# Kernel tuning notes

Hardware: AMD Instinct MI355X
Metric: run time of the kernel (lower is better)

The kernel has to match this reference:

```python
import jax, jax.numpy as jnp
from jax import lax
import numpy as np

C_IN, C_OUT, K, STRIDE = 256, 512, 3, 1
EPS = 1e-5


def setup_inputs() -> dict:
    key = jax.random.key(0)
    ks = jax.random.split(key, 8)
    B, H, W = 32, 56, 56
    x = jax.random.normal(ks[0], (B, C_IN, H, W), dtype=jnp.float32)
    dw_w = jax.random.normal(ks[1], (C_IN, 1, K, K), dtype=jnp.float32) * 0.1
    dw_b = jax.random.normal(ks[2], (C_IN,), dtype=jnp.float32) * 0.05
    g1 = jnp.ones((C_IN,), dtype=jnp.float32)
    b1 = jnp.zeros((C_IN,), dtype=jnp.float32)
    pw_w = jax.random.normal(ks[3], (C_OUT, C_IN), dtype=jnp.float32) * (1.0 / np.sqrt(C_IN))
    pw_b = jax.random.normal(ks[4], (C_OUT,), dtype=jnp.float32) * 0.05
    g2 = jnp.ones((C_OUT,), dtype=jnp.float32)
    b2 = jnp.zeros((C_OUT,), dtype=jnp.float32)
    return {"x": x, "dw_w": dw_w, "dw_b": dw_b, "g1": g1, "b1": b1,
            "pw_w": pw_w, "pw_b": pw_b, "g2": g2, "b2": b2}


def _batchnorm(x, gamma, beta):
    # training-mode BN over (N, H, W) per channel, matching fresh nn.BatchNorm2d
    mean = jnp.mean(x, axis=(0, 2, 3), keepdims=True)
    var = jnp.var(x, axis=(0, 2, 3), keepdims=True)
    xn = (x - mean) * lax.rsqrt(var + EPS)
    return xn * gamma[None, :, None, None] + beta[None, :, None, None]


def reference(x, dw_w, dw_b, g1, b1, pw_w, pw_b, g2, b2):
    p = K // 2
    # reflect padding (padding_mode='reflect' in torch Conv2d)
    xp = jnp.pad(x, ((0, 0), (0, 0), (p, p), (p, p)), mode='reflect')
    # grouped depthwise conv: one filter per channel
    y = lax.conv_general_dilated(
        xp, dw_w, window_strides=(STRIDE, STRIDE), padding='VALID',
        dimension_numbers=('NCHW', 'OIHW', 'NCHW'),
        feature_group_count=C_IN)
    y = y + dw_b[None, :, None, None]
    y = jax.nn.relu(_batchnorm(y, g1, b1))
    # pointwise 1x1 conv == channel GEMM
    z = jnp.einsum('bchw,oc->bohw', y, pw_w) + pw_b[None, :, None, None]
    z = jax.nn.relu(_batchnorm(z, g2, b2))
    return z
```

## Files before the change

kernel.cpp:

```cpp
#include <hip/hip_runtime.h>
#include <hip/hip_bf16.h>
#include <stdint.h>


#define CIN   256
#define COUT  512
#define BATCH 32
#define HH    56
#define WWID  56
#define HWSZ  3136
#define NTOT  100352
#define NHWF  100352.0f
#define EPSV  1e-5f

typedef __bf16 bf16;
typedef __bf16 bf16x8 __attribute__((ext_vector_type(8)));
typedef float  f32x4  __attribute__((ext_vector_type(4)));

#define WS_STATS1   0
#define WS_SCALE1   2048
#define WS_SHIFT1   3072
#define WS_STATS2   4096
#define WS_WBF      16384
#define WS_YT       278528
#define WS_ZBF      51658752

__device__ __forceinline__ void gload16(const void* g, void* l) {
  __builtin_amdgcn_global_load_lds((const __attribute__((address_space(1))) void*)g,
                                   (__attribute__((address_space(3))) void*)l, 16, 0, 0);
}
__device__ __forceinline__ float bfu(unsigned int u16) {
  unsigned int x = u16 << 16;
  return __builtin_bit_cast(float, x);
}

__global__ __launch_bounds__(256) void k1_dwstats(const float* __restrict__ x,
                                                  const float* __restrict__ dww,
                                                  float* __restrict__ stats1) {
  __shared__ float plane[HWSZ];
  __shared__ float red[8];
  int bid = blockIdx.x;
  int c = bid & (CIN - 1);
  int b = bid >> 8;
  const float4* xp4 = (const float4*)(x + ((size_t)(b * CIN + c)) * HWSZ);
  float4* pl4 = (float4*)plane;
  for (int i = threadIdx.x; i < HWSZ / 4; i += 256) pl4[i] = xp4[i];
  float w9[9];
#pragma unroll
  for (int q = 0; q < 9; ++q) w9[q] = dww[c * 9 + q];
  __syncthreads();
  float s = 0.f, sq = 0.f;
  for (int p = threadIdx.x; p < HWSZ; p += 256) {
    int h = p / WWID;
    int w = p - h * WWID;
    float acc = 0.f;
#pragma unroll
    for (int dy = 0; dy < 3; ++dy) {
      int hh = h - 1 + dy;
      hh = hh < 0 ? 1 : (hh > 55 ? 54 : hh);
#pragma unroll
      for (int dx = 0; dx < 3; ++dx) {
        int ww2 = w - 1 + dx;
        ww2 = ww2 < 0 ? 1 : (ww2 > 55 ? 54 : ww2);
        acc += w9[dy * 3 + dx] * plane[hh * WWID + ww2];
      }
    }
    s += acc; sq += acc * acc;
  }
#pragma unroll
  for (int m = 1; m < 64; m <<= 1) { s += __shfl_xor(s, m); sq += __shfl_xor(sq, m); }
  int wv = threadIdx.x >> 6;
  if ((threadIdx.x & 63) == 0) { red[wv] = s; red[4 + wv] = sq; }
  __syncthreads();
  if (threadIdx.x == 0) {
    atomicAdd(&stats1[c],        red[0] + red[1] + red[2] + red[3]);
    atomicAdd(&stats1[CIN + c],  red[4] + red[5] + red[6] + red[7]);
  }
}

__global__ __launch_bounds__(256) void k2_finalize1(const float* __restrict__ stats1,
                                                    const float* __restrict__ g1,
                                                    const float* __restrict__ b1,
                                                    const float* __restrict__ pww,
                                                    float* __restrict__ scale1,
                                                    float* __restrict__ shift1,
                                                    bf16* __restrict__ wbf) {
  int blk = blockIdx.x, t = threadIdx.x;
  if (blk == 0) {
    float mean = stats1[t] * (1.0f / NHWF);
    float var  = stats1[CIN + t] * (1.0f / NHWF) - mean * mean;
    float sc = g1[t] * rsqrtf(var + EPSV);
    scale1[t] = sc;
    shift1[t] = b1[t] - mean * sc;
  } else {
    int o = blk - 1;
    wbf[o * CIN + t] = (bf16)pww[o * CIN + t];
  }
}

__global__ __launch_bounds__(256) void k3_normT(const float* __restrict__ x,
                                                const float* __restrict__ dww,
                                                const float* __restrict__ scale1,
                                                const float* __restrict__ shift1,
                                                bf16* __restrict__ yt) {
  __shared__ float xt[64][3][58];
  __shared__ __align__(16) bf16 outt[56][64];
  int bid = blockIdx.x;
  int cg = bid & 3;
  int h  = (bid >> 2) % 56;
  int b  = bid / 224;
  int c0 = cg * 64;
  int hr0 = (h == 0) ? 1 : h - 1;
  int hr2 = (h == 55) ? 54 : h + 1;
  for (int idx = threadIdx.x; idx < 64 * 3 * 56; idx += 256) {
    int c = idx / 168;
    int rem = idx - c * 168;
    int r = rem / 56;
    int w = rem - r * 56;
    int hr = (r == 0) ? hr0 : ((r == 1) ? h : hr2);
    xt[c][r][w + 1] = x[((size_t)((b * CIN + c0 + c) * HH + hr)) * WWID + w];
  }
  __syncthreads();
  if (threadIdx.x < 192) {
    int c = threadIdx.x / 3, r = threadIdx.x % 3;
    xt[c][r][0]  = xt[c][r][2];
    xt[c][r][57] = xt[c][r][55];
  }
  __syncthreads();
  int c  = threadIdx.x >> 2;
  int wq = threadIdx.x & 3;
  float w9[9];
#pragma unroll
  for (int q = 0; q < 9; ++q) w9[q] = dww[(c0 + c) * 9 + q];
  float sc = scale1[c0 + c], sh = shift1[c0 + c];
  for (int w = wq; w < 56; w += 4) {
    float acc = 0.f;
#pragma unroll
    for (int r = 0; r < 3; ++r) {
      const float* row = &xt[c][r][w];
      acc += w9[r * 3 + 0] * row[0] + w9[r * 3 + 1] * row[1] + w9[r * 3 + 2] * row[2];
    }
    float v = fmaxf(acc * sc + sh, 0.f);
    outt[w][c] = (bf16)v;
  }
  __syncthreads();
  for (int idx = threadIdx.x; idx < 56 * 8; idx += 256) {
    int w = idx >> 3, part = idx & 7;
    uint4 v = *(const uint4*)(&outt[w][part * 8]);
    *(uint4*)(yt + ((size_t)(b * HWSZ + h * WWID + w)) * CIN + c0 + part * 8) = v;
  }
}

__global__ __launch_bounds__(256) void k4_gemm(const bf16* __restrict__ wbf,
                                               const bf16* __restrict__ yt,
                                               bf16* __restrict__ zbf,
                                               float* __restrict__ stats2) {
  __shared__ __align__(16) unsigned char LDSBUF[32768];
  __shared__ float sl[256];
  unsigned char* Als = LDSBUF;
  unsigned char* Bls = LDSBUF + 16384;
  int wg = blockIdx.x;
  int newid = (wg & 7) * 392 + (wg >> 3);
  int mt    = newid & 3;
  int ntile = newid >> 2;
  int tid = threadIdx.x;
  int wv = tid >> 6, l = tid & 63;
  int wm = wv >> 1, wn = wv & 1;
  f32x4 acc[4][4];
#pragma unroll
  for (int mi = 0; mi < 4; ++mi)
#pragma unroll
    for (int ni = 0; ni < 4; ++ni) acc[mi][ni] = (f32x4){0.f, 0.f, 0.f, 0.f};
  const char* wb = (const char*)wbf;
  const char* yb = (const char*)yt + (size_t)ntile * 128 * CIN * 2;

  for (int k0 = 0; k0 < 256; k0 += 64) {
#pragma unroll
    for (int i = 0; i < 4; ++i) {
      int q = i * 256 + wv * 64 + l;
      int row = q >> 3, pp = q & 7;
      int cc = pp ^ (row & 7);
      gload16(wb + ((size_t)(mt * 128 + row) * CIN + k0) * 2 + cc * 16,
              Als + i * 4096 + wv * 1024);
      gload16(yb + ((size_t)row * CIN + k0) * 2 + cc * 16,
              Bls + i * 4096 + wv * 1024);
    }
    __syncthreads();
#pragma unroll
    for (int kk = 0; kk < 2; ++kk) {
      bf16x8 af[4], bfr[4];
#pragma unroll
      for (int mi = 0; mi < 4; ++mi) {
        int row = wm * 64 + mi * 16 + (l & 15);
        int ck = kk * 4 + (l >> 4);
        af[mi] = *(const bf16x8*)(Als + row * 128 + ((ck ^ (row & 7)) << 4));
      }
#pragma unroll
      for (int ni = 0; ni < 4; ++ni) {
        int row = wn * 64 + ni * 16 + (l & 15);
        int ck = kk * 4 + (l >> 4);
        bfr[ni] = *(const bf16x8*)(Bls + row * 128 + ((ck ^ (row & 7)) << 4));
      }
#pragma unroll
      for (int mi = 0; mi < 4; ++mi)
#pragma unroll
        for (int ni = 0; ni < 4; ++ni)
          acc[mi][ni] = __builtin_amdgcn_mfma_f32_16x16x32_bf16(af[mi], bfr[ni], acc[mi][ni], 0, 0, 0);
    }
    __syncthreads();
  }

  sl[tid] = 0.f;
  __syncthreads();
#pragma unroll
  for (int mi = 0; mi < 4; ++mi)
#pragma unroll
    for (int j = 0; j < 4; ++j) {
      float s = 0.f, q2 = 0.f;
#pragma unroll
      for (int ni = 0; ni < 4; ++ni) {
        float v = acc[mi][ni][j];
        s += v; q2 += v * v;
      }
#pragma unroll
      for (int m = 1; m < 16; m <<= 1) { s += __shfl_xor(s, m); q2 += __shfl_xor(q2, m); }
      if ((l & 15) == 0) {
        int ol = wm * 64 + mi * 16 + (l >> 4) * 4 + j;
        atomicAdd(&sl[ol], s);
        atomicAdd(&sl[128 + ol], q2);
      }
    }
  __syncthreads();
  {
    int which = tid >> 7, i = tid & 127;
    atomicAdd(&stats2[which * COUT + mt * 128 + i], sl[tid]);
  }

  bf16* zl = (bf16*)LDSBUF;
#pragma unroll
  for (int mi = 0; mi < 4; ++mi)
#pragma unroll
    for (int ni = 0; ni < 4; ++ni)
#pragma unroll
      for (int j = 0; j < 4; ++j) {
        int ol = wm * 64 + mi * 16 + (l >> 4) * 4 + j;
        int rl = wn * 64 + ni * 16 + (l & 15);
        zl[ol * 128 + rl] = (bf16)acc[mi][ni][j];
      }
  __syncthreads();
  size_t rbase = (size_t)ntile * 128;
  for (int ch = tid; ch < 2048; ch += 256) {
    int ol = ch >> 4, r8 = ch & 15;
    size_t r = rbase + (size_t)r8 * 8;
    int b  = (int)(r / HWSZ);
    int hw = (int)(r - (size_t)b * HWSZ);
    int o  = mt * 128 + ol;
    *(uint4*)(zbf + ((size_t)(b * COUT + o)) * HWSZ + hw) = *(const uint4*)(zl + ol * 128 + r8 * 8);
  }
}

__global__ __launch_bounds__(256) void k5_bn2(const bf16* __restrict__ zbf,
                                              const float* __restrict__ stats2,
                                              const float* __restrict__ g2,
                                              const float* __restrict__ b2,
                                              float* __restrict__ out) {
  __shared__ float s2l[COUT], sh2l[COUT];
  for (int c = threadIdx.x; c < COUT; c += 256) {
    float mean = stats2[c] * (1.0f / NHWF);
    float var  = stats2[COUT + c] * (1.0f / NHWF) - mean * mean;
    float sc = g2[c] * rsqrtf(var + EPSV);
    s2l[c]  = sc;
    sh2l[c] = b2[c] - mean * sc;
  }
  __syncthreads();
  const int n8 = BATCH * COUT * HWSZ / 8;
  int stride = gridDim.x * blockDim.x;
  const uint4* z4 = (const uint4*)zbf;
  for (int i = blockIdx.x * blockDim.x + threadIdx.x; i < n8; i += stride) {
    int c = (i / 392) & (COUT - 1);
    float s = s2l[c], sh = sh2l[c];
    uint4 v = z4[i];
    float4 o1, o2;
    o1.x = fmaxf(bfu(v.x & 0xffffu) * s + sh, 0.f);
    o1.y = fmaxf(bfu(v.x >> 16)     * s + sh, 0.f);
    o1.z = fmaxf(bfu(v.y & 0xffffu) * s + sh, 0.f);
    o1.w = fmaxf(bfu(v.y >> 16)     * s + sh, 0.f);
    o2.x = fmaxf(bfu(v.z & 0xffffu) * s + sh, 0.f);
    o2.y = fmaxf(bfu(v.z >> 16)     * s + sh, 0.f);
    o2.z = fmaxf(bfu(v.w & 0xffffu) * s + sh, 0.f);
    o2.w = fmaxf(bfu(v.w >> 16)     * s + sh, 0.f);
    *(float4*)(out + (size_t)i * 8)     = o1;
    *(float4*)(out + (size_t)i * 8 + 4) = o2;
  }
}

extern "C" void kernel_launch(void* const* d_in, const int* in_sizes, int n_in,
                              void* d_out, int out_size, void* d_ws, size_t ws_size,
                              hipStream_t stream) {
  const float* x   = (const float*)d_in[0];
  const float* dww = (const float*)d_in[1];
  const float* g1  = (const float*)d_in[3];
  const float* b1  = (const float*)d_in[4];
  const float* pww = (const float*)d_in[5];
  const float* g2  = (const float*)d_in[7];
  const float* b2  = (const float*)d_in[8];
  float* out = (float*)d_out;
  char* ws = (char*)d_ws;
  float* stats1 = (float*)(ws + WS_STATS1);
  float* scale1 = (float*)(ws + WS_SCALE1);
  float* shift1 = (float*)(ws + WS_SHIFT1);
  float* stats2 = (float*)(ws + WS_STATS2);
  bf16* wbf = (bf16*)(ws + WS_WBF);
  bf16* yt  = (bf16*)(ws + WS_YT);
  bf16* zbf = (bf16*)(ws + WS_ZBF);

  hipMemsetAsync(d_ws, 0, 8192, stream);
  k1_dwstats<<<BATCH * CIN, 256, 0, stream>>>(x, dww, stats1);
  k2_finalize1<<<513, 256, 0, stream>>>(stats1, g1, b1, pww, scale1, shift1, wbf);
  k3_normT<<<BATCH * 56 * 4, 256, 0, stream>>>(x, dww, scale1, shift1, yt);
  k4_gemm<<<3136, 256, 0, stream>>>(wbf, yt, zbf, stats2);
  k5_bn2<<<2048, 256, 0, stream>>>(zbf, stats2, g2, b2, out);
}
```

Baseline: 502.6 us.

## Compute BN2 statistics analytically via Gram matrix, fuse BN2+ReLU into GEMM epilogue

```diff
diff --git a/kernel.cpp b/kernel.cpp
--- a/kernel.cpp
+++ b/kernel.cpp
@@ -20,18 +20,16 @@
 #define WS_STATS1   0
 #define WS_SCALE1   2048
 #define WS_SHIFT1   3072
-#define WS_STATS2   4096
-#define WS_WBF      16384
-#define WS_YT       278528
-#define WS_ZBF      51658752
+#define WS_YSUM     4096
+#define WS_S2       5120
+#define WS_T2       7168
+#define WS_G        16384
+#define WS_WBF      278528
+#define WS_YT       540672
 
 __device__ __forceinline__ void gload16(const void* g, void* l) {
   __builtin_amdgcn_global_load_lds((const __attribute__((address_space(1))) void*)g,
                                    (__attribute__((address_space(3))) void*)l, 16, 0, 0);
-}
-__device__ __forceinline__ float bfu(unsigned int u16) {
-  unsigned int x = u16 << 16;
-  return __builtin_bit_cast(float, x);
 }
 
 __global__ __launch_bounds__(256) void k1_dwstats(const float* __restrict__ x,
@@ -151,12 +149,118 @@
   }
 }
 
+__global__ __launch_bounds__(256) void kg_gram(const bf16* __restrict__ yt,
+                                               float* __restrict__ G,
+                                               float* __restrict__ ysum) {
+  __shared__ __align__(16) unsigned short yTl[256 * 64];
+  int bid = blockIdx.x;
+  int job = bid & 3;
+  int chunk = bid >> 2;
+  int qa = job >> 1, qb = job & 1;
+  int tid = threadIdx.x;
+  int wv = tid >> 6, l = tid & 63;
+  int wm = wv >> 1, wn = wv & 1;
+  f32x4 acc[4][4];
+#pragma unroll
+  for (int mi = 0; mi < 4; ++mi)
+#pragma unroll
+    for (int ni = 0; ni < 4; ++ni) acc[mi][ni] = (f32x4){0.f, 0.f, 0.f, 0.f};
+  float ys = 0.f;
+  int r_loc = tid >> 2;
+  int ci0 = tid & 3;
+  int rs_k[8];
+#pragma unroll
+  for (int k = 0; k < 8; ++k) rs_k[k] = (r_loc & 7) | (((r_loc >> 3) ^ k) << 3);
+
+  for (int it = 0; it < 16; ++it) {
+    const unsigned short* src = (const unsigned short*)yt + ((size_t)chunk * 1024 + it * 64 + r_loc) * CIN;
+#pragma unroll
+    for (int u = 0; u < 8; ++u) {
+      int c0 = (ci0 + u * 4) * 8;
+      unsigned short v8[8];
+      *(uint4*)v8 = *(const uint4*)(src + c0);
+#pragma unroll
+      for (int k = 0; k < 8; ++k) yTl[(c0 + k) * 64 + rs_k[k]] = v8[k];
+    }
+    __syncthreads();
+#pragma unroll
+    for (int kk = 0; kk < 2; ++kk) {
+      bf16x8 af[4], bfr[4];
+      int rc = kk * 4 + (l >> 4);
+#pragma unroll
+      for (int mi = 0; mi < 4; ++mi) {
+        int c = qa * 128 + wm * 64 + mi * 16 + (l & 15);
+        af[mi] = *(const bf16x8*)(yTl + c * 64 + ((rc ^ (c & 7)) << 3));
+      }
+#pragma unroll
+      for (int ni = 0; ni < 4; ++ni) {
+        int c = qb * 128 + wn * 64 + ni * 16 + (l & 15);
+        bfr[ni] = *(const bf16x8*)(yTl + c * 64 + ((rc ^ (c & 7)) << 3));
+      }
+#pragma unroll
+      for (int mi = 0; mi < 4; ++mi)
+#pragma unroll
+        for (int ni = 0; ni < 4; ++ni)
+          acc[mi][ni] = __builtin_amdgcn_mfma_f32_16x16x32_bf16(af[mi], bfr[ni], acc[mi][ni], 0, 0, 0);
+    }
+    if (job == 0) {
+      const bf16* row = (const bf16*)(yTl + tid * 64);
+#pragma unroll
+      for (int i = 0; i < 64; ++i) ys += (float)row[i];
+    }
+    __syncthreads();
+  }
+#pragma unroll
+  for (int mi = 0; mi < 4; ++mi)
+#pragma unroll
+    for (int ni = 0; ni < 4; ++ni)
+#pragma unroll
+      for (int j = 0; j < 4; ++j) {
+        int m = qa * 128 + wm * 64 + mi * 16 + (l >> 4) * 4 + j;
+        int n = qb * 128 + wn * 64 + ni * 16 + (l & 15);
+        atomicAdd(&G[m * 256 + n], acc[mi][ni][j]);
+      }
+  if (job == 0) atomicAdd(&ysum[tid], ys);
+}
+
+__global__ __launch_bounds__(256) void k2c_fin2(const float* __restrict__ G,
+                                                const float* __restrict__ ysum,
+                                                const bf16* __restrict__ wbf,
+                                                const float* __restrict__ g2,
+                                                const float* __restrict__ b2,
+                                                float* __restrict__ s2,
+                                                float* __restrict__ t2) {
+  __shared__ float wl[256];
+  __shared__ float red[8];
+  int o = blockIdx.x, t = threadIdx.x;
+  wl[t] = (float)wbf[o * 256 + t];
+  __syncthreads();
+  float gw = 0.f;
+  for (int c = 0; c < 256; ++c) gw += G[c * 256 + t] * wl[c];
+  float msq_p  = gw * wl[t];
+  float mean_p = wl[t] * ysum[t];
+#pragma unroll
+  for (int m = 1; m < 64; m <<= 1) { msq_p += __shfl_xor(msq_p, m); mean_p += __shfl_xor(mean_p, m); }
+  int wv = t >> 6;
+  if ((t & 63) == 0) { red[wv] = msq_p; red[4 + wv] = mean_p; }
+  __syncthreads();
+  if (t == 0) {
+    float msq  = (red[0] + red[1] + red[2] + red[3]) * (1.0f / NHWF);
+    float mean = (red[4] + red[5] + red[6] + red[7]) * (1.0f / NHWF);
+    float var  = msq - mean * mean;
+    float sc = g2[o] * rsqrtf(var + EPSV);
+    s2[o] = sc;
+    t2[o] = b2[o] - mean * sc;
+  }
+}
+
 __global__ __launch_bounds__(256) void k4_gemm(const bf16* __restrict__ wbf,
                                                const bf16* __restrict__ yt,
-                                               bf16* __restrict__ zbf,
-                                               float* __restrict__ stats2) {
+                                               const float* __restrict__ s2,
+                                               const float* __restrict__ t2,
+                                               float* __restrict__ out) {
   __shared__ __align__(16) unsigned char LDSBUF[32768];
-  __shared__ float sl[256];
+  __shared__ float s2l[128], t2l[128];
   unsigned char* Als = LDSBUF;
   unsigned char* Bls = LDSBUF + 16384;
   int wg = blockIdx.x;
@@ -166,6 +270,7 @@
   int tid = threadIdx.x;
   int wv = tid >> 6, l = tid & 63;
   int wm = wv >> 1, wn = wv & 1;
+  if (tid < 128) { s2l[tid] = s2[mt * 128 + tid]; t2l[tid] = t2[mt * 128 + tid]; }
   f32x4 acc[4][4];
 #pragma unroll
   for (int mi = 0; mi < 4; ++mi)
@@ -210,33 +315,6 @@
     __syncthreads();
   }
 
-  sl[tid] = 0.f;
-  __syncthreads();
-#pragma unroll
-  for (int mi = 0; mi < 4; ++mi)
-#pragma unroll
-    for (int j = 0; j < 4; ++j) {
-      float s = 0.f, q2 = 0.f;
-#pragma unroll
-      for (int ni = 0; ni < 4; ++ni) {
-        float v = acc[mi][ni][j];
-        s += v; q2 += v * v;
-      }
-#pragma unroll
-      for (int m = 1; m < 16; m <<= 1) { s += __shfl_xor(s, m); q2 += __shfl_xor(q2, m); }
-      if ((l & 15) == 0) {
-        int ol = wm * 64 + mi * 16 + (l >> 4) * 4 + j;
-        atomicAdd(&sl[ol], s);
-        atomicAdd(&sl[128 + ol], q2);
-      }
-    }
-  __syncthreads();
-  {
-    int which = tid >> 7, i = tid & 127;
-    atomicAdd(&stats2[which * COUT + mt * 128 + i], sl[tid]);
-  }
-
-  bf16* zl = (bf16*)LDSBUF;
 #pragma unroll
   for (int mi = 0; mi < 4; ++mi)
 #pragma unroll
@@ -244,54 +322,12 @@
 #pragma unroll
       for (int j = 0; j < 4; ++j) {
         int ol = wm * 64 + mi * 16 + (l >> 4) * 4 + j;
-        int rl = wn * 64 + ni * 16 + (l & 15);
-        zl[ol * 128 + rl] = (bf16)acc[mi][ni][j];
-      }
-  __syncthreads();
-  size_t rbase = (size_t)ntile * 128;
-  for (int ch = tid; ch < 2048; ch += 256) {
-    int ol = ch >> 4, r8 = ch & 15;
-    size_t r = rbase + (size_t)r8 * 8;
-    int b  = (int)(r / HWSZ);
-    int hw = (int)(r - (size_t)b * HWSZ);
-    int o  = mt * 128 + ol;
-    *(uint4*)(zbf + ((size_t)(b * COUT + o)) * HWSZ + hw) = *(const uint4*)(zl + ol * 128 + r8 * 8);
-  }
-}
-
-__global__ __launch_bounds__(256) void k5_bn2(const bf16* __restrict__ zbf,
-                                              const float* __restrict__ stats2,
-                                              const float* __restrict__ g2,
-                                              const float* __restrict__ b2,
-                                              float* __restrict__ out) {
-  __shared__ float s2l[COUT], sh2l[COUT];
-  for (int c = threadIdx.x; c < COUT; c += 256) {
-    float mean = stats2[c] * (1.0f / NHWF);
-    float var  = stats2[COUT + c] * (1.0f / NHWF) - mean * mean;
-    float sc = g2[c] * rsqrtf(var + EPSV);
-    s2l[c]  = sc;
-    sh2l[c] = b2[c] - mean * sc;
-  }
-  __syncthreads();
-  const int n8 = BATCH * COUT * HWSZ / 8;
-  int stride = gridDim.x * blockDim.x;
-  const uint4* z4 = (const uint4*)zbf;
-  for (int i = blockIdx.x * blockDim.x + threadIdx.x; i < n8; i += stride) {
-    int c = (i / 392) & (COUT - 1);
-    float s = s2l[c], sh = sh2l[c];
-    uint4 v = z4[i];
-    float4 o1, o2;
-    o1.x = fmaxf(bfu(v.x & 0xffffu) * s + sh, 0.f);
-    o1.y = fmaxf(bfu(v.x >> 16)     * s + sh, 0.f);
-    o1.z = fmaxf(bfu(v.y & 0xffffu) * s + sh, 0.f);
-    o1.w = fmaxf(bfu(v.y >> 16)     * s + sh, 0.f);
-    o2.x = fmaxf(bfu(v.z & 0xffffu) * s + sh, 0.f);
-    o2.y = fmaxf(bfu(v.z >> 16)     * s + sh, 0.f);
-    o2.z = fmaxf(bfu(v.w & 0xffffu) * s + sh, 0.f);
-    o2.w = fmaxf(bfu(v.w >> 16)     * s + sh, 0.f);
-    *(float4*)(out + (size_t)i * 8)     = o1;
-    *(float4*)(out + (size_t)i * 8 + 4) = o2;
-  }
+        int r_flat = ntile * 128 + wn * 64 + ni * 16 + (l & 15);
+        int b  = r_flat / HWSZ;
+        int hw = r_flat - b * HWSZ;
+        float v = fmaxf(acc[mi][ni][j] * s2l[ol] + t2l[ol], 0.f);
+        out[((size_t)(b * COUT + mt * 128 + ol)) * HWSZ + hw] = v;
+      }
 }
 
 extern "C" void kernel_launch(void* const* d_in, const int* in_sizes, int n_in,
@@ -309,15 +345,18 @@
   float* stats1 = (float*)(ws + WS_STATS1);
   float* scale1 = (float*)(ws + WS_SCALE1);
   float* shift1 = (float*)(ws + WS_SHIFT1);
-  float* stats2 = (float*)(ws + WS_STATS2);
+  float* ysum   = (float*)(ws + WS_YSUM);
+  float* s2     = (float*)(ws + WS_S2);
+  float* t2     = (float*)(ws + WS_T2);
+  float* G      = (float*)(ws + WS_G);
   bf16* wbf = (bf16*)(ws + WS_WBF);
   bf16* yt  = (bf16*)(ws + WS_YT);
-  bf16* zbf = (bf16*)(ws + WS_ZBF);
-
-  hipMemsetAsync(d_ws, 0, 8192, stream);
+
+  hipMemsetAsync(d_ws, 0, WS_WBF, stream);
   k1_dwstats<<<BATCH * CIN, 256, 0, stream>>>(x, dww, stats1);
   k2_finalize1<<<513, 256, 0, stream>>>(stats1, g1, b1, pww, scale1, shift1, wbf);
   k3_normT<<<BATCH * 56 * 4, 256, 0, stream>>>(x, dww, scale1, shift1, yt);
-  k4_gemm<<<3136, 256, 0, stream>>>(wbf, yt, zbf, stats2);
-  k5_bn2<<<2048, 256, 0, stream>>>(zbf, stats2, g2, b2, out);
-}
+  kg_gram<<<392, 256, 0, stream>>>(yt, G, ysum);
+  k2c_fin2<<<COUT, 256, 0, stream>>>(G, ysum, wbf, g2, b2, s2, t2);
+  k4_gemm<<<3136, 256, 0, stream>>>(wbf, yt, s2, t2, out);
+}
```

After: 499.9 us. Within noise of the previous version (-0.5%).
